# Optimization experiments

Measured on AMD Instinct MI355X. Metric: run time of the kernel, lower is better.

The kernel has to match this reference:

```python
import jax, jax.numpy as jnp
import numpy as np

B, N, C = 8, 8192, 512
H, DH = 8, C // 8
SCALE = 0.02


def setup_inputs() -> dict:
    key = jax.random.key(0)
    k0, k1, k2, k3, k4 = jax.random.split(key, 5)
    return {
        "x": jax.random.normal(k0, (B, N, C), dtype=jnp.float32),
        "w1": SCALE * jax.random.normal(k1, (2, H, DH, DH), dtype=jnp.float32),
        "b1": SCALE * jax.random.normal(k2, (2, H, DH), dtype=jnp.float32),
        "w2": SCALE * jax.random.normal(k3, (2, H, DH, DH), dtype=jnp.float32),
        "b2": SCALE * jax.random.normal(k4, (2, H, DH), dtype=jnp.float32),
    }


def reference(x, w1, b1, w2, b2):
    dtype = x.dtype
    x = x.astype(jnp.float32)
    b, n, c = x.shape
    xf = jnp.fft.rfft(x, axis=1, norm="ortho")            # [B, N//2+1, C] complex
    xf = xf.reshape(b, n // 2 + 1, H, DH)                  # [B, F, H, DH]
    xr, xi = jnp.real(xf), jnp.imag(xf)
    # per-head complex linear 1 + GELU (complex mult split into real/imag)
    o1r = jax.nn.gelu(
        jnp.einsum("bfhi,hio->bfho", xr, w1[0])
        - jnp.einsum("bfhi,hio->bfho", xi, w1[1]) + b1[0], approximate=False)
    o1i = jax.nn.gelu(
        jnp.einsum("bfhi,hio->bfho", xi, w1[0])
        + jnp.einsum("bfhi,hio->bfho", xr, w1[1]) + b1[1], approximate=False)
    # per-head complex linear 2
    o2r = (jnp.einsum("bfhi,hio->bfho", o1r, w2[0])
           - jnp.einsum("bfhi,hio->bfho", o1i, w2[1]) + b2[0])
    o2i = (jnp.einsum("bfhi,hio->bfho", o1i, w2[0])
           + jnp.einsum("bfhi,hio->bfho", o1r, w2[1]) + b2[1])
    yf = (o2r + 1j * o2i).reshape(b, n // 2 + 1, c)
    y = jnp.fft.irfft(yf, n=n, axis=1, norm="ortho")
    return y.astype(dtype)
```

## Files before the change

### kernel.cpp

```cpp
#include <hip/hip_runtime.h>
#include <math.h>

#define BB    8
#define NLEN  8192
#define CC    512
#define HH    8
#define DH    64
#define MH    4096
#define FREQ  4097
#define FP    4104
#define NSEQ  (BB*CC)

#define REGION_BYTES ((size_t)NSEQ * FP * 4ull)

static __device__ __align__(256) unsigned char g_scratch[2ull * (size_t)NSEQ * FP * 4ull];
__device__ unsigned short g_wprep[8 * 4 * 64 * 64];

typedef __attribute__((ext_vector_type(8))) short bf16x8;
typedef __attribute__((ext_vector_type(4))) float f32x4;

__device__ __forceinline__ f32x4 MFMA(bf16x8 a, bf16x8 b, f32x4 c){
  return __builtin_amdgcn_mfma_f32_16x16x32_bf16(a, b, c, 0, 0, 0);
}

__device__ __forceinline__ unsigned short f2bf(float f){
  unsigned u = __float_as_uint(f);
  return (unsigned short)((u + 0x7fffu + ((u >> 16) & 1u)) >> 16);
}
__device__ __forceinline__ unsigned pack2(float a, float b){
  return (unsigned)f2bf(a) | ((unsigned)f2bf(b) << 16);
}
__device__ __forceinline__ float bflo(unsigned u){ return __uint_as_float(u << 16); }
__device__ __forceinline__ float bfhi(unsigned u){ return __uint_as_float(u & 0xffff0000u); }

__device__ __forceinline__ void async_ld16(const unsigned* g, unsigned* l){
  __builtin_amdgcn_global_load_lds(
      (const __attribute__((address_space(1))) unsigned*)g,
      (__attribute__((address_space(3))) unsigned*)l, 16, 0, 0);
}

__device__ const float C32C[16] = {
  1.f, 0.98078528f, 0.92387953f, 0.83146961f, 0.70710678f, 0.55557023f,
  0.38268343f, 0.19509032f, 0.f, -0.19509032f, -0.38268343f, -0.55557023f,
  -0.70710678f, -0.83146961f, -0.92387953f, -0.98078528f};
__device__ const float C32S[16] = {
  0.f, 0.19509032f, 0.38268343f, 0.55557023f, 0.70710678f, 0.83146961f,
  0.92387953f, 0.98078528f, 1.f, 0.98078528f, 0.92387953f, 0.83146961f,
  0.70710678f, 0.55557023f, 0.38268343f, 0.19509032f};

__device__ __forceinline__ float gelu_fast(float v){
  float x  = v * 0.70710678118654752440f;
  float ax = fabsf(x);
  float t  = __builtin_amdgcn_rcpf(fmaf(0.3275911f, ax, 1.0f));
  float p  = fmaf(fmaf(fmaf(fmaf(1.061405429f, t, -1.453152027f), t,
                            1.421413741f), t, -0.284496736f), t, 0.254829592f);
  float e  = __expf(-x * x);
  float erf_ax = fmaf(-p * t, e, 1.0f);
  float erfx = copysignf(erf_ax, x);
  return 0.5f * v * (1.0f + erfx);
}

__device__ __forceinline__ float2 cadd(float2 a, float2 b){ return make_float2(a.x+b.x, a.y+b.y); }
__device__ __forceinline__ float2 csub(float2 a, float2 b){ return make_float2(a.x-b.x, a.y-b.y); }
__device__ __forceinline__ float2 cmul(float2 a, float2 b){
  return make_float2(fmaf(a.x, b.x, -(a.y*b.y)), fmaf(a.x, b.y, a.y*b.x));
}

__global__ __launch_bounds__(256) void transpose_in_k(const float* __restrict__ in,
                                                      unsigned* __restrict__ out){
  __shared__ float tile[64][33];
  int b  = blockIdx.z;
  int c0 = blockIdx.x * 32;
  int n0 = blockIdx.y * 64;
  int t  = threadIdx.x;
  int tx = t & 31, ty = t >> 5;
  const float* src = in + ((size_t)b * NLEN + n0) * CC + c0;
  #pragma unroll
  for (int k = 0; k < 8; ++k)
    tile[ty + 8*k][tx] = src[(size_t)(ty + 8*k) * CC + tx];
  __syncthreads();
  int lt = t & 15;
  int nl = 4 * lt;
  #pragma unroll
  for (int kk = 0; kk < 2; ++kk){
    int cl = (t >> 4) + 16*kk;
    uint2 u;
    u.x = pack2(tile[nl    ][cl], tile[nl + 1][cl]);
    u.y = pack2(tile[nl + 2][cl], tile[nl + 3][cl]);
    *(uint2*)(out + ((size_t)(b * CC + c0 + cl) * NLEN + n0) / 2 + 2*lt) = u;
  }
}

__global__ __launch_bounds__(256) void transpose_out_k(const unsigned* __restrict__ in,
                                                       float* __restrict__ out){
  __shared__ float tile[64][33];
  int b  = blockIdx.z;
  int c0 = blockIdx.x * 32;
  int n0 = blockIdx.y * 64;
  int t  = threadIdx.x;
  int lt = t & 15;
  int nl = 4 * lt;
  #pragma unroll
  for (int kk = 0; kk < 2; ++kk){
    int cl = (t >> 4) + 16*kk;
    uint2 u = *(const uint2*)(in + ((size_t)(b * CC + c0 + cl) * NLEN + n0) / 2 + 2*lt);
    tile[nl    ][cl] = bflo(u.x);
    tile[nl + 1][cl] = bfhi(u.x);
    tile[nl + 2][cl] = bflo(u.y);
    tile[nl + 3][cl] = bfhi(u.y);
  }
  __syncthreads();
  int tx = t & 31, ty = t >> 5;
  float* dst = out + ((size_t)b * NLEN + n0) * CC + c0;
  #pragma unroll
  for (int k = 0; k < 8; ++k)
    dst[(size_t)(ty + 8*k) * CC + tx] = tile[ty + 8*k][tx];
}

#define SL(e) ((e) + ((e) >> 4))
#define PERM16(p) ((((p) & 3) << 2) | ((p) >> 2))

template<int SIGN>
__device__ __forceinline__ void dft4ip(float2& v0, float2& v1, float2& v2, float2& v3){
  float2 s02 = cadd(v0, v2), d02 = csub(v0, v2);
  float2 s13 = cadd(v1, v3), d13 = csub(v1, v3);
  float2 id = make_float2(-(float)SIGN * d13.y, (float)SIGN * d13.x);
  v0 = cadd(s02, s13);
  v1 = cadd(d02, id);
  v2 = csub(s02, s13);
  v3 = csub(d02, id);
}

template<int SIGN>
__device__ __forceinline__ float2 w16c(int m){
  const float c1 = 0.9238795325112867f, s1 = 0.3826834323650898f, r = 0.7071067811865476f;
  float cs = 1.f, sn = 0.f;
  if (m == 1){ cs = c1;  sn = s1; }
  else if (m == 2){ cs = r;   sn = r; }
  else if (m == 3){ cs = s1;  sn = c1; }
  else if (m == 4){ cs = 0.f; sn = 1.f; }
  else if (m == 6){ cs = -r;  sn = r; }
  else if (m == 9){ cs = -c1; sn = -s1; }
  return make_float2(cs, (float)SIGN * sn);
}

template<int SIGN>
__device__ __forceinline__ void dft16ip(float2 v[16]){
  #pragma unroll
  for (int q0 = 0; q0 < 4; ++q0) dft4ip<SIGN>(v[q0], v[q0+4], v[q0+8], v[q0+12]);
  #pragma unroll
  for (int p0 = 0; p0 < 4; ++p0)
    #pragma unroll
    for (int q0 = 0; q0 < 4; ++q0){
      const int m = p0 * q0;
      if (m) v[q0 + 4*p0] = cmul(v[q0 + 4*p0], w16c<SIGN>(m));
    }
  #pragma unroll
  for (int p0 = 0; p0 < 4; ++p0) dft4ip<SIGN>(v[4*p0], v[4*p0+1], v[4*p0+2], v[4*p0+3]);
}

template<int SIGN>
__device__ __forceinline__ void twiddle16(float2 v[16], int jm, float invRNs){
  float ang = (float)SIGN * 6.2831853071795864769f * (float)jm * invRNs;
  float sn, cs; __sincosf(ang, &sn, &cs);
  float2 tw[16];
  tw[1] = make_float2(cs, sn);
  #pragma unroll
  for (int q = 2; q < 16; ++q) tw[q] = cmul(tw[q >> 1], tw[q - (q >> 1)]);
  #pragma unroll
  for (int q = 1; q < 16; ++q) v[q] = cmul(v[q], tw[q]);
}

template<int SIGN, int NS>
__device__ __forceinline__ void fft_mid_pass(float2* lds2, float2 v[16], int t){
  #pragma unroll
  for (int q = 0; q < 16; ++q) v[q] = lds2[SL(t + 256*q)];
  int jm = t & (NS - 1);
  twiddle16<SIGN>(v, jm, 1.0f / (16.0f * (float)NS));
  dft16ip<SIGN>(v);
  __syncthreads();
  int base = ((t - jm) << 4) + jm;
  #pragma unroll
  for (int p = 0; p < 16; ++p) lds2[SL(base + p*NS)] = v[PERM16(p)];
  __syncthreads();
}

#define ORTHO_S 0.011048543456039806f

__global__ __launch_bounds__(256) void fft_fwd_k(const unsigned* __restrict__ xt,
                                                 unsigned* __restrict__ spec){
  __shared__ float2 lds2[4352];
  int t = threadIdx.x;
  size_t row = blockIdx.x;
  const unsigned* src = xt + row * (NLEN/2);
  float2 v[16];
  #pragma unroll
  for (int q = 0; q < 16; ++q){
    unsigned u = src[t + 256*q];
    v[q] = make_float2(bflo(u), bfhi(u));
  }
  dft16ip<-1>(v);
  #pragma unroll
  for (int p = 0; p < 16; ++p) lds2[SL(16*t + p)] = v[PERM16(p)];
  __syncthreads();
  fft_mid_pass<-1, 16 >(lds2, v, t);
  fft_mid_pass<-1, 256>(lds2, v, t);
  unsigned* dst = spec + row * (size_t)FP;
  float snb, csb;
  __sincosf(-6.2831853071795864769f * (float)t / (float)NLEN, &snb, &csb);
  #pragma unroll
  for (int q = 0; q < 16; ++q){
    int k = t + 256*q;
    float2 zk = lds2[SL(k)];
    float2 zc = lds2[SL((MH - k) & (MH - 1))];
    float ex = 0.5f*(zk.x + zc.x);
    float ey = 0.5f*(zk.y - zc.y);
    float ux = zk.x - zc.x;
    float uy = zk.y + zc.y;
    float ox =  0.5f*uy;
    float oy = -0.5f*ux;
    float cs = fmaf(csb, C32C[q],  snb*C32S[q]);
    float sn = fmaf(snb, C32C[q], -csb*C32S[q]);
    float xr = ex + cs*ox - sn*oy;
    float xi = ey + cs*oy + sn*ox;
    dst[k] = pack2(ORTHO_S*xr, ORTHO_S*xi);
  }
  if (t == 0){
    float2 z0 = lds2[SL(0)];
    dst[MH] = pack2(ORTHO_S*(z0.x - z0.y), 0.0f);
  }
}

__global__ __launch_bounds__(256) void fft_inv_k(const unsigned* __restrict__ spec,
                                                 unsigned* __restrict__ yt){
  __shared__ float2 lds2[4352];
  int t = threadIdx.x;
  size_t row = blockIdx.x;
  const unsigned* src = spec + row * (size_t)FP;
  float2 v[16];
  float snb, csb;
  __sincosf(6.2831853071795864769f * (float)t / (float)NLEN, &snb, &csb);
  #pragma unroll
  for (int q = 0; q < 16; ++q){
    int k = t + 256*q;
    unsigned uk = src[k];
    unsigned uc = src[MH - k];
    float2 xk = make_float2(bflo(uk), bfhi(uk));
    float2 xc = make_float2(bflo(uc), bfhi(uc));
    if (k == 0){ xk.y = 0.0f; xc.y = 0.0f; }
    float ex = xk.x + xc.x;
    float ey = xk.y - xc.y;
    float dx = xk.x - xc.x;
    float dy = xk.y + xc.y;
    float cs = fmaf(csb, C32C[q], -snb*C32S[q]);
    float sn = fmaf(snb, C32C[q],  csb*C32S[q]);
    float ox = cs*dx - sn*dy;
    float oy = cs*dy + sn*dx;
    v[q] = make_float2(ex - oy, ey + ox);
  }
  dft16ip<1>(v);
  #pragma unroll
  for (int p = 0; p < 16; ++p) lds2[SL(16*t + p)] = v[PERM16(p)];
  __syncthreads();
  fft_mid_pass<1, 16 >(lds2, v, t);
  fft_mid_pass<1, 256>(lds2, v, t);
  unsigned* dst = yt + row * (NLEN/2);
  #pragma unroll
  for (int q = 0; q < 16; ++q){
    int m = t + 256*q;
    float2 w = lds2[SL(m)];
    dst[m] = pack2(ORTHO_S*w.x, ORTHO_S*w.y);
  }
}

__global__ __launch_bounds__(256) void wprep_k(const float* __restrict__ w1,
                                               const float* __restrict__ w2){
  int t = threadIdx.x;
  int h = blockIdx.x;
  #pragma unroll 4
  for (int u = 0; u < 64; ++u){
    int idx = t + 256*u;
    int p = idx >> 12;
    int o = (idx >> 6) & 63;
    int jj = idx & 63;
    int swo = (o ^ (o >> 3)) & 7;
    int s = (((jj >> 3) ^ swo) << 3) | (jj & 7);
    int i;
    if (p < 2){
      i = s;
    } else {
      int ks = s >> 5, g = (s >> 3) & 3, j = s & 7;
      i = (2*ks + (j >> 2))*16 + 4*g + (j & 3);
    }
    const float* src = (p < 2) ? w1 : w2;
    float v = src[(size_t)(p & 1) * 32768 + (size_t)h * 4096 + i * 64 + o];
    g_wprep[(size_t)h * 16384 + idx] = f2bf(v);
  }
}

__global__ __launch_bounds__(256) void afno_mid_mfma_k(const unsigned* __restrict__ spec_in,
                                                       unsigned* __restrict__ spec_out,
                                                       const float* __restrict__ b1,
                                                       const float* __restrict__ b2){
  __shared__ __align__(16) unsigned char smem[65536];
  unsigned short* Wl = (unsigned short*)smem;
  const int t = threadIdx.x;
  const int chunk = blockIdx.x, h = blockIdx.y, b = blockIdx.z;
  const int ntiles = (chunk == 7) ? 9 : 8;
  const int tb = chunk * 8;
  const size_t rowbase = ((size_t)b * HH + h) * DH;
  const int l = t & 63, wv = t >> 6;
  const int lf = l & 15, lg = l >> 4;
  const int wf0 = wv * 16;
  const int grow = l >> 4, gfq = l & 15;

  {
    const uint4* gw  = (const uint4*)(g_wprep + (size_t)h * 16384);
    uint4*       sw4 = (uint4*)smem;
    #pragma unroll
    for (int u = 0; u < 8; ++u) sw4[t + 256*u] = gw[t + 256*u];
  }
  float4 br1[4], bi1[4];
  #pragma unroll
  for (int mt = 0; mt < 4; ++mt){
    br1[mt] = *(const float4*)(b1 +       (size_t)h*64 + mt*16 + lg*4);
    bi1[mt] = *(const float4*)(b1 + 512 + (size_t)h*64 + mt*16 + lg*4);
  }
  float b2r[4], b2i[4];
  #pragma unroll
  for (int nt = 0; nt < 4; ++nt){
    b2r[nt] = b2[(size_t)h*64 + nt*16 + lf];
    b2i[nt] = b2[512 + (size_t)h*64 + nt*16 + lf];
  }

  auto STAGE = [&](int tt){
    unsigned char* xb = smem + 32768 + ((tt & 1) << 14);
    int F0 = (tb + tt) * 64;
    int fu = F0 + gfq * 4;
    if (fu > FP - 4) fu = FP - 4;
    #pragma unroll
    for (int g2 = 0; g2 < 4; ++g2){
      int g = wv * 4 + g2;
      const unsigned* gs = spec_in + (rowbase + g*4 + grow) * (size_t)FP + fu;
      async_ld16(gs, (unsigned*)(xb + g * 1024));
    }
  };

  STAGE(0);
  __syncthreads();

  const unsigned short* W1R = Wl;
  const unsigned short* W1I = Wl + 4096;
  const unsigned short* W2R = Wl + 8192;
  const unsigned short* W2I = Wl + 12288;
  const f32x4 zz = {0.f, 0.f, 0.f, 0.f};

  for (int tt = 0; tt < ntiles; ++tt){
    if (tt + 1 < ntiles) STAGE(tt + 1);
    const unsigned char* xb = smem + 32768 + ((tt & 1) << 14);
    const unsigned char* xlane = xb + lg*2048 + (wf0 + lf)*4;
    const int F0 = (tb + tt) * 64;

    f32x4 a1R[4], a1I[4];
    #pragma unroll
    for (int mt = 0; mt < 4; ++mt){ a1R[mt] = zz; a1I[mt] = zz; }

    #pragma unroll
    for (int ks = 0; ks < 2; ++ks){
      unsigned bins[8];
      #pragma unroll
      for (int j = 0; j < 8; ++j)
        bins[j] = *(const unsigned*)(xlane + ks*8192 + j*256);
      bf16x8 bxr, bxi;
      {
        unsigned* pr = (unsigned*)&bxr;
        unsigned* pi = (unsigned*)&bxi;
        #pragma unroll
        for (int w = 0; w < 4; ++w){
          pr[w] = __builtin_amdgcn_perm(bins[2*w+1], bins[2*w], 0x05040100u);
          pi[w] = __builtin_amdgcn_perm(bins[2*w+1], bins[2*w], 0x07060302u);
        }
      }
      int b0 = ks*4 + lg;
      #pragma unroll
      for (int mt = 0; mt < 4; ++mt){
        int o = mt*16 + lf;
        int swo = (o ^ (o >> 3)) & 7;
        int off = o*64 + ((b0 ^ swo) << 3);
        bf16x8 awr  = *(const bf16x8*)(W1R + off);
        bf16x8 awi  = *(const bf16x8*)(W1I + off);
        bf16x8 awin = awi ^ (short)0x8000;
        a1R[mt] = MFMA(awr,  bxr, a1R[mt]);
        a1R[mt] = MFMA(awin, bxi, a1R[mt]);
        a1I[mt] = MFMA(awi,  bxr, a1I[mt]);
        a1I[mt] = MFMA(awr,  bxi, a1I[mt]);
      }
    }

    bf16x8 aFr[2], aFi[2], aFin[2];
    #pragma unroll
    for (int ks = 0; ks < 2; ++ks){
      unsigned wr_[4], wi_[4];
      #pragma unroll
      for (int half = 0; half < 2; ++half){
        int mt = 2*ks + half;
        float vr0 = gelu_fast(a1R[mt][0] + br1[mt].x), vr1 = gelu_fast(a1R[mt][1] + br1[mt].y);
        float vr2 = gelu_fast(a1R[mt][2] + br1[mt].z), vr3 = gelu_fast(a1R[mt][3] + br1[mt].w);
        float vi0 = gelu_fast(a1I[mt][0] + bi1[mt].x), vi1 = gelu_fast(a1I[mt][1] + bi1[mt].y);
        float vi2 = gelu_fast(a1I[mt][2] + bi1[mt].z), vi3 = gelu_fast(a1I[mt][3] + bi1[mt].w);
        wr_[half*2    ] = pack2(vr0, vr1);
        wr_[half*2 + 1] = pack2(vr2, vr3);
        wi_[half*2    ] = pack2(vi0, vi1);
        wi_[half*2 + 1] = pack2(vi2, vi3);
      }
      unsigned* pr = (unsigned*)&aFr[ks];
      unsigned* pi = (unsigned*)&aFi[ks];
      #pragma unroll
      for (int w = 0; w < 4; ++w){ pr[w] = wr_[w]; pi[w] = wi_[w]; }
      aFin[ks] = aFi[ks] ^ (short)0x8000;
    }

    f32x4 a2R[4], a2I[4];
    #pragma unroll
    for (int nt = 0; nt < 4; ++nt){ a2R[nt] = zz; a2I[nt] = zz; }
    #pragma unroll
    for (int ks = 0; ks < 2; ++ks){
      int b0 = ks*4 + lg;
      #pragma unroll
      for (int nt = 0; nt < 4; ++nt){
        int o2 = nt*16 + lf;
        int swo = (o2 ^ (o2 >> 3)) & 7;
        int off = o2*64 + ((b0 ^ swo) << 3);
        bf16x8 bwr = *(const bf16x8*)(W2R + off);
        bf16x8 bwi = *(const bf16x8*)(W2I + off);
        a2R[nt] = MFMA(aFr[ks],  bwr, a2R[nt]);
        a2R[nt] = MFMA(aFin[ks], bwi, a2R[nt]);
        a2I[nt] = MFMA(aFi[ks],  bwr, a2I[nt]);
        a2I[nt] = MFMA(aFr[ks],  bwi, a2I[nt]);
      }
    }

    int f0 = F0 + wf0 + lg*4;
    if (f0 <= MH){
      #pragma unroll
      for (int nt = 0; nt < 4; ++nt){
        int o2 = nt*16 + lf;
        uint4 st;
        st.x = pack2(a2R[nt][0] + b2r[nt], a2I[nt][0] + b2i[nt]);
        st.y = pack2(a2R[nt][1] + b2r[nt], a2I[nt][1] + b2i[nt]);
        st.z = pack2(a2R[nt][2] + b2r[nt], a2I[nt][2] + b2i[nt]);
        st.w = pack2(a2R[nt][3] + b2r[nt], a2I[nt][3] + b2i[nt]);
        *(uint4*)(spec_out + (rowbase + o2) * (size_t)FP + f0) = st;
      }
    }
    __syncthreads();
  }
}

extern "C" void kernel_launch(void* const* d_in, const int* in_sizes, int n_in,
                              void* d_out, int out_size, void* d_ws, size_t ws_size,
                              hipStream_t stream) {
  const float* x  = (const float*)d_in[0];
  const float* w1 = (const float*)d_in[1];
  const float* b1 = (const float*)d_in[2];
  const float* w2 = (const float*)d_in[3];
  const float* b2 = (const float*)d_in[4];
  float* out = (float*)d_out;

  unsigned char* base = (unsigned char*)d_ws;
  if (ws_size < 2 * REGION_BYTES){
    void* p = nullptr;
    hipGetSymbolAddress(&p, HIP_SYMBOL(g_scratch));
    base = (unsigned char*)p;
  }
  unsigned* specA = (unsigned*)base;
  unsigned char* regB = base + REGION_BYTES;
  unsigned* xt    = (unsigned*)regB;
  unsigned* specB = (unsigned*)regB;
  unsigned* ytp   = (unsigned*)base;

  wprep_k<<<8, 256, 0, stream>>>(w1, w2);
  transpose_in_k<<<dim3(CC/32, NLEN/64, BB), 256, 0, stream>>>(x, xt);
  fft_fwd_k<<<NSEQ, 256, 0, stream>>>(xt, specA);
  afno_mid_mfma_k<<<dim3(8, HH, BB), 256, 0, stream>>>(specA, specB, b1, b2);
  fft_inv_k<<<NSEQ, 256, 0, stream>>>(specB, ytp);
  transpose_out_k<<<dim3(CC/32, NLEN/64, BB), 256, 0, stream>>>(ytp, out);
}
```

Before: 212.5 us.

## Launch one block per frequency tile and load spectra directly into registers

```diff
diff --git a/kernel.cpp b/kernel.cpp
--- a/kernel.cpp
+++ b/kernel.cpp
@@ -32,12 +32,6 @@
 }
 __device__ __forceinline__ float bflo(unsigned u){ return __uint_as_float(u << 16); }
 __device__ __forceinline__ float bfhi(unsigned u){ return __uint_as_float(u & 0xffff0000u); }
-
-__device__ __forceinline__ void async_ld16(const unsigned* g, unsigned* l){
-  __builtin_amdgcn_global_load_lds(
-      (const __attribute__((address_space(1))) unsigned*)g,
-      (__attribute__((address_space(3))) unsigned*)l, 16, 0, 0);
-}
 
 __device__ const float C32C[16] = {
   1.f, 0.98078528f, 0.92387953f, 0.83146961f, 0.70710678f, 0.55557023f,
@@ -302,21 +296,30 @@
                                                        unsigned* __restrict__ spec_out,
                                                        const float* __restrict__ b1,
                                                        const float* __restrict__ b2){
-  __shared__ __align__(16) unsigned char smem[65536];
-  unsigned short* Wl = (unsigned short*)smem;
+  __shared__ unsigned short Wl[16384];
   const int t = threadIdx.x;
-  const int chunk = blockIdx.x, h = blockIdx.y, b = blockIdx.z;
-  const int ntiles = (chunk == 7) ? 9 : 8;
-  const int tb = chunk * 8;
+  const int bx = blockIdx.x, h = blockIdx.y, b = blockIdx.z;
+  const int F0 = bx * 64;
   const size_t rowbase = ((size_t)b * HH + h) * DH;
   const int l = t & 63, wv = t >> 6;
   const int lf = l & 15, lg = l >> 4;
   const int wf0 = wv * 16;
-  const int grow = l >> 4, gfq = l & 15;
+
+  int f = F0 + wf0 + lf;
+  int fc = (f < FP) ? f : (FP - 1);
+  const unsigned* xcol = spec_in + rowbase * (size_t)FP + fc;
+  unsigned bins[2][8];
+  #pragma unroll
+  for (int ks = 0; ks < 2; ++ks){
+    int i0 = (ks*4 + lg) * 8;
+    #pragma unroll
+    for (int j = 0; j < 8; ++j)
+      bins[ks][j] = xcol[(i0 + j) * FP];
+  }
 
   {
     const uint4* gw  = (const uint4*)(g_wprep + (size_t)h * 16384);
-    uint4*       sw4 = (uint4*)smem;
+    uint4*       sw4 = (uint4*)Wl;
     #pragma unroll
     for (int u = 0; u < 8; ++u) sw4[t + 256*u] = gw[t + 256*u];
   }
@@ -332,21 +335,6 @@
     b2r[nt] = b2[(size_t)h*64 + nt*16 + lf];
     b2i[nt] = b2[512 + (size_t)h*64 + nt*16 + lf];
   }
-
-  auto STAGE = [&](int tt){
-    unsigned char* xb = smem + 32768 + ((tt & 1) << 14);
-    int F0 = (tb + tt) * 64;
-    int fu = F0 + gfq * 4;
-    if (fu > FP - 4) fu = FP - 4;
-    #pragma unroll
-    for (int g2 = 0; g2 < 4; ++g2){
-      int g = wv * 4 + g2;
-      const unsigned* gs = spec_in + (rowbase + g*4 + grow) * (size_t)FP + fu;
-      async_ld16(gs, (unsigned*)(xb + g * 1024));
-    }
-  };
-
-  STAGE(0);
   __syncthreads();
 
   const unsigned short* W1R = Wl;
@@ -355,105 +343,93 @@
   const unsigned short* W2I = Wl + 12288;
   const f32x4 zz = {0.f, 0.f, 0.f, 0.f};
 
-  for (int tt = 0; tt < ntiles; ++tt){
-    if (tt + 1 < ntiles) STAGE(tt + 1);
-    const unsigned char* xb = smem + 32768 + ((tt & 1) << 14);
-    const unsigned char* xlane = xb + lg*2048 + (wf0 + lf)*4;
-    const int F0 = (tb + tt) * 64;
-
-    f32x4 a1R[4], a1I[4];
-    #pragma unroll
-    for (int mt = 0; mt < 4; ++mt){ a1R[mt] = zz; a1I[mt] = zz; }
-
-    #pragma unroll
-    for (int ks = 0; ks < 2; ++ks){
-      unsigned bins[8];
+  f32x4 a1R[4], a1I[4];
+  #pragma unroll
+  for (int mt = 0; mt < 4; ++mt){ a1R[mt] = zz; a1I[mt] = zz; }
+
+  #pragma unroll
+  for (int ks = 0; ks < 2; ++ks){
+    bf16x8 bxr, bxi;
+    {
+      unsigned* pr = (unsigned*)&bxr;
+      unsigned* pi = (unsigned*)&bxi;
       #pragma unroll
-      for (int j = 0; j < 8; ++j)
-        bins[j] = *(const unsigned*)(xlane + ks*8192 + j*256);
-      bf16x8 bxr, bxi;
-      {
-        unsigned* pr = (unsigned*)&bxr;
-        unsigned* pi = (unsigned*)&bxi;
-        #pragma unroll
-        for (int w = 0; w < 4; ++w){
-          pr[w] = __builtin_amdgcn_perm(bins[2*w+1], bins[2*w], 0x05040100u);
-          pi[w] = __builtin_amdgcn_perm(bins[2*w+1], bins[2*w], 0x07060302u);
-        }
+      for (int w = 0; w < 4; ++w){
+        pr[w] = __builtin_amdgcn_perm(bins[ks][2*w+1], bins[ks][2*w], 0x05040100u);
+        pi[w] = __builtin_amdgcn_perm(bins[ks][2*w+1], bins[ks][2*w], 0x07060302u);
       }
-      int b0 = ks*4 + lg;
-      #pragma unroll
-      for (int mt = 0; mt < 4; ++mt){
-        int o = mt*16 + lf;
-        int swo = (o ^ (o >> 3)) & 7;
-        int off = o*64 + ((b0 ^ swo) << 3);
-        bf16x8 awr  = *(const bf16x8*)(W1R + off);
-        bf16x8 awi  = *(const bf16x8*)(W1I + off);
-        bf16x8 awin = awi ^ (short)0x8000;
-        a1R[mt] = MFMA(awr,  bxr, a1R[mt]);
-        a1R[mt] = MFMA(awin, bxi, a1R[mt]);
-        a1I[mt] = MFMA(awi,  bxr, a1I[mt]);
-        a1I[mt] = MFMA(awr,  bxi, a1I[mt]);
-      }
-    }
-
-    bf16x8 aFr[2], aFi[2], aFin[2];
-    #pragma unroll
-    for (int ks = 0; ks < 2; ++ks){
-      unsigned wr_[4], wi_[4];
-      #pragma unroll
-      for (int half = 0; half < 2; ++half){
-        int mt = 2*ks + half;
-        float vr0 = gelu_fast(a1R[mt][0] + br1[mt].x), vr1 = gelu_fast(a1R[mt][1] + br1[mt].y);
-        float vr2 = gelu_fast(a1R[mt][2] + br1[mt].z), vr3 = gelu_fast(a1R[mt][3] + br1[mt].w);
-        float vi0 = gelu_fast(a1I[mt][0] + bi1[mt].x), vi1 = gelu_fast(a1I[mt][1] + bi1[mt].y);
-        float vi2 = gelu_fast(a1I[mt][2] + bi1[mt].z), vi3 = gelu_fast(a1I[mt][3] + bi1[mt].w);
-        wr_[half*2    ] = pack2(vr0, vr1);
-        wr_[half*2 + 1] = pack2(vr2, vr3);
-        wi_[half*2    ] = pack2(vi0, vi1);
-        wi_[half*2 + 1] = pack2(vi2, vi3);
-      }
-      unsigned* pr = (unsigned*)&aFr[ks];
-      unsigned* pi = (unsigned*)&aFi[ks];
-      #pragma unroll
-      for (int w = 0; w < 4; ++w){ pr[w] = wr_[w]; pi[w] = wi_[w]; }
-      aFin[ks] = aFi[ks] ^ (short)0x8000;
-    }
-
-    f32x4 a2R[4], a2I[4];
-    #pragma unroll
-    for (int nt = 0; nt < 4; ++nt){ a2R[nt] = zz; a2I[nt] = zz; }
-    #pragma unroll
-    for (int ks = 0; ks < 2; ++ks){
-      int b0 = ks*4 + lg;
-      #pragma unroll
-      for (int nt = 0; nt < 4; ++nt){
-        int o2 = nt*16 + lf;
-        int swo = (o2 ^ (o2 >> 3)) & 7;
-        int off = o2*64 + ((b0 ^ swo) << 3);
-        bf16x8 bwr = *(const bf16x8*)(W2R + off);
-        bf16x8 bwi = *(const bf16x8*)(W2I + off);
-        a2R[nt] = MFMA(aFr[ks],  bwr, a2R[nt]);
-        a2R[nt] = MFMA(aFin[ks], bwi, a2R[nt]);
-        a2I[nt] = MFMA(aFi[ks],  bwr, a2I[nt]);
-        a2I[nt] = MFMA(aFr[ks],  bwi, a2I[nt]);
-      }
-    }
-
-    int f0 = F0 + wf0 + lg*4;
-    if (f0 <= MH){
-      #pragma unroll
-      for (int nt = 0; nt < 4; ++nt){
-        int o2 = nt*16 + lf;
-        uint4 st;
-        st.x = pack2(a2R[nt][0] + b2r[nt], a2I[nt][0] + b2i[nt]);
-        st.y = pack2(a2R[nt][1] + b2r[nt], a2I[nt][1] + b2i[nt]);
-        st.z = pack2(a2R[nt][2] + b2r[nt], a2I[nt][2] + b2i[nt]);
-        st.w = pack2(a2R[nt][3] + b2r[nt], a2I[nt][3] + b2i[nt]);
-        *(uint4*)(spec_out + (rowbase + o2) * (size_t)FP + f0) = st;
-      }
-    }
-    __syncthreads();
+    }
+    int b0 = ks*4 + lg;
+    #pragma unroll
+    for (int mt = 0; mt < 4; ++mt){
+      int o = mt*16 + lf;
+      int swo = (o ^ (o >> 3)) & 7;
+      int off = o*64 + ((b0 ^ swo) << 3);
+      bf16x8 awr  = *(const bf16x8*)(W1R + off);
+      bf16x8 awi  = *(const bf16x8*)(W1I + off);
+      bf16x8 awin = awi ^ (short)0x8000;
+      a1R[mt] = MFMA(awr,  bxr, a1R[mt]);
+      a1R[mt] = MFMA(awin, bxi, a1R[mt]);
+      a1I[mt] = MFMA(awi,  bxr, a1I[mt]);
+      a1I[mt] = MFMA(awr,  bxi, a1I[mt]);
+    }
+  }
+
+  bf16x8 aFr[2], aFi[2], aFin[2];
+  #pragma unroll
+  for (int ks = 0; ks < 2; ++ks){
+    unsigned wr_[4], wi_[4];
+    #pragma unroll
+    for (int half = 0; half < 2; ++half){
+      int mt = 2*ks + half;
+      float vr0 = gelu_fast(a1R[mt][0] + br1[mt].x), vr1 = gelu_fast(a1R[mt][1] + br1[mt].y);
+      float vr2 = gelu_fast(a1R[mt][2] + br1[mt].z), vr3 = gelu_fast(a1R[mt][3] + br1[mt].w);
+      float vi0 = gelu_fast(a1I[mt][0] + bi1[mt].x), vi1 = gelu_fast(a1I[mt][1] + bi1[mt].y);
+      float vi2 = gelu_fast(a1I[mt][2] + bi1[mt].z), vi3 = gelu_fast(a1I[mt][3] + bi1[mt].w);
+      wr_[half*2    ] = pack2(vr0, vr1);
+      wr_[half*2 + 1] = pack2(vr2, vr3);
+      wi_[half*2    ] = pack2(vi0, vi1);
+      wi_[half*2 + 1] = pack2(vi2, vi3);
+    }
+    unsigned* pr = (unsigned*)&aFr[ks];
+    unsigned* pi = (unsigned*)&aFi[ks];
+    #pragma unroll
+    for (int w = 0; w < 4; ++w){ pr[w] = wr_[w]; pi[w] = wi_[w]; }
+    aFin[ks] = aFi[ks] ^ (short)0x8000;
+  }
+
+  f32x4 a2R[4], a2I[4];
+  #pragma unroll
+  for (int nt = 0; nt < 4; ++nt){ a2R[nt] = zz; a2I[nt] = zz; }
+  #pragma unroll
+  for (int ks = 0; ks < 2; ++ks){
+    int b0 = ks*4 + lg;
+    #pragma unroll
+    for (int nt = 0; nt < 4; ++nt){
+      int o2 = nt*16 + lf;
+      int swo = (o2 ^ (o2 >> 3)) & 7;
+      int off = o2*64 + ((b0 ^ swo) << 3);
+      bf16x8 bwr = *(const bf16x8*)(W2R + off);
+      bf16x8 bwi = *(const bf16x8*)(W2I + off);
+      a2R[nt] = MFMA(aFr[ks],  bwr, a2R[nt]);
+      a2R[nt] = MFMA(aFin[ks], bwi, a2R[nt]);
+      a2I[nt] = MFMA(aFi[ks],  bwr, a2I[nt]);
+      a2I[nt] = MFMA(aFr[ks],  bwi, a2I[nt]);
+    }
+  }
+
+  int f0 = F0 + wf0 + lg*4;
+  if (f0 <= MH){
+    #pragma unroll
+    for (int nt = 0; nt < 4; ++nt){
+      int o2 = nt*16 + lf;
+      uint4 st;
+      st.x = pack2(a2R[nt][0] + b2r[nt], a2I[nt][0] + b2i[nt]);
+      st.y = pack2(a2R[nt][1] + b2r[nt], a2I[nt][1] + b2i[nt]);
+      st.z = pack2(a2R[nt][2] + b2r[nt], a2I[nt][2] + b2i[nt]);
+      st.w = pack2(a2R[nt][3] + b2r[nt], a2I[nt][3] + b2i[nt]);
+      *(uint4*)(spec_out + (rowbase + o2) * (size_t)FP + f0) = st;
+    }
   }
 }
 
@@ -482,7 +458,7 @@
   wprep_k<<<8, 256, 0, stream>>>(w1, w2);
   transpose_in_k<<<dim3(CC/32, NLEN/64, BB), 256, 0, stream>>>(x, xt);
   fft_fwd_k<<<NSEQ, 256, 0, stream>>>(xt, specA);
-  afno_mid_mfma_k<<<dim3(8, HH, BB), 256, 0, stream>>>(specA, specB, b1, b2);
+  afno_mid_mfma_k<<<dim3(65, HH, BB), 256, 0, stream>>>(specA, specB, b1, b2);
   fft_inv_k<<<NSEQ, 256, 0, stream>>>(specB, ytp);
   transpose_out_k<<<dim3(CC/32, NLEN/64, BB), 256, 0, stream>>>(ytp, out);
 }
```

After: 211.1 us. No clear change (-0.7%).
